# Kernel optimization log

Measured on AMD Instinct MI355X. Metric: run time of the kernel, lower is better.

Reference implementation:

```python
import jax, jax.numpy as jnp
import numpy as np

NUM_HEADS = 8
NUM_POINTS = 4


def _bilinear_gather(vl, loc, h, w):
    """MSDeformAttn bilinear sampling (align_corners=False, zero padding).
    vl: (BN, h*w, H, D) one level's values; loc: (BN, Q, H, P, 2) normalized [0,1].
    Returns (BN, Q, H, P, D)."""
    BN, _, H, D = vl.shape
    Q, P = loc.shape[1], loc.shape[3]
    x = loc[..., 0] * w - 0.5
    y = loc[..., 1] * h - 0.5
    x0 = jnp.floor(x); y0 = jnp.floor(y)
    lx = x - x0; ly = y - y0
    x0i = x0.astype(jnp.int32); y0i = y0.astype(jnp.int32)
    x1i = x0i + 1; y1i = y0i + 1
    vt = vl.transpose(0, 2, 1, 3)  # (BN, H, hw, D)

    def gather(yi, xi):
        valid = (yi >= 0) & (yi < h) & (xi >= 0) & (xi < w)
        idx = jnp.clip(yi, 0, h - 1) * w + jnp.clip(xi, 0, w - 1)  # (BN,Q,H,P)
        idx_t = idx.transpose(0, 2, 1, 3).reshape(BN, H, Q * P)
        g = jnp.take_along_axis(vt, idx_t[..., None], axis=2)  # (BN,H,QP,D)
        g = g.reshape(BN, H, Q, P, D).transpose(0, 2, 1, 3, 4)
        return jnp.where(valid[..., None], g, jnp.zeros((), vl.dtype))

    w00 = ((1 - ly) * (1 - lx))[..., None]
    w01 = ((1 - ly) * lx)[..., None]
    w10 = (ly * (1 - lx))[..., None]
    w11 = (ly * lx)[..., None]
    return (gather(y0i, x0i) * w00 + gather(y0i, x1i) * w01
            + gather(y1i, x0i) * w10 + gather(y1i, x1i) * w11)


def _forward(query, value, reference_points, query_mask, spatial_shapes, level_start_index,
             Wv, bv, Woff, boff, Watt, batt, Wo, bo):
    B, Z, Y, X, C = query.shape
    Q = Z * Y * X
    BN = value.shape[0]
    N = BN // B  # cameras per sample (uniform lengths)
    H, P = NUM_HEADS, NUM_POINTS
    shapes = np.asarray(spatial_shapes)  # static level shapes
    starts = np.asarray(level_start_index)
    L = shapes.shape[0]
    D = C // H
    mask = query_mask.astype(query.dtype)  # (BN, Q)
    # expand each sample's voxel queries to its N cameras
    qf = jnp.broadcast_to(query.reshape(B, 1, Q, C), (B, N, Q, C)).reshape(BN, Q, C)
    v = (value @ Wv + bv).reshape(BN, -1, H, D)
    off = (qf @ Woff + boff).reshape(BN, Q, H, L, P, 2)
    aw = jax.nn.softmax((qf @ Watt + batt).reshape(BN, Q, H, L * P), axis=-1)
    aw = aw.reshape(BN, Q, H, L, P)
    # offset_normalizer = (w, h) per level
    normalizer = jnp.asarray(np.stack([shapes[:, 1], shapes[:, 0]], -1), query.dtype)
    loc = reference_points[:, :, None, None, None, :] + off / normalizer[None, None, None, :, None, :]
    out = jnp.zeros((BN, Q, H, D), query.dtype)
    for l in range(L):
        h, w = int(shapes[l, 0]), int(shapes[l, 1])
        s = int(starts[l])
        vl = v[:, s:s + h * w]
        sampled = _bilinear_gather(vl, loc[:, :, :, l], h, w)  # (BN,Q,H,P,D)
        out = out + jnp.einsum('bqhpd,bqhp->bqhd', sampled, aw[:, :, :, l])
    attn = out.reshape(BN, Q, C) @ Wo + bo
    # identity + attn, then rebatch_mask_sequence zeroes non-masked voxels
    full = (qf + attn) * mask[..., None]
    summed = full.reshape(B, N, Q, C).sum(axis=1)
    counts = jnp.maximum(mask.reshape(B, N, Q).sum(axis=1), 1.0)
    return (summed / counts[..., None]).reshape(B, Z, Y, X, C)


def setup_inputs() -> dict:
    key = jax.random.key(0)
    ks = jax.random.split(key, 9)
    B, N = 2, 4
    Z, Y, X, C = 8, 32, 32, 256
    Q = Z * Y * X
    BN = B * N
    shapes = np.array([[64, 112], [32, 56], [16, 28], [8, 14]], np.int64)
    starts = np.concatenate([[0], np.cumsum(shapes[:, 0] * shapes[:, 1])[:-1]]).astype(np.int64)
    Nv = int((shapes[:, 0] * shapes[:, 1]).sum())  # 9520
    H, L, P = NUM_HEADS, shapes.shape[0], NUM_POINTS
    s = 0.02
    return dict(
        query=jax.random.normal(ks[0], (B, Z, Y, X, C), jnp.float32),
        value=jax.random.normal(ks[1], (BN, Nv, C), jnp.float32),
        reference_points=jax.random.uniform(ks[2], (BN, Q, 2), jnp.float32),
        query_mask=jax.random.bernoulli(ks[3], 0.6, (BN, Q)),
        spatial_shapes=jnp.asarray(shapes),
        level_start_index=jnp.asarray(starts),
        Wv=jax.random.normal(ks[4], (C, C), jnp.float32) * s,
        bv=jnp.zeros((C,), jnp.float32),
        Woff=jax.random.normal(ks[5], (C, H * L * P * 2), jnp.float32) * s,
        boff=jax.random.normal(ks[6], (H * L * P * 2,), jnp.float32),
        Watt=jax.random.normal(ks[7], (C, H * L * P), jnp.float32) * s,
        batt=jnp.zeros((H * L * P,), jnp.float32),
        Wo=jax.random.normal(ks[8], (C, C), jnp.float32) * s,
        bo=jnp.zeros((C,), jnp.float32),
    )


def reference(query, value, reference_points, query_mask, spatial_shapes, level_start_index,
              Wv, bv, Woff, boff, Watt, batt, Wo, bo):
    return _forward(query, value, reference_points, query_mask, spatial_shapes, level_start_index,
                    Wv, bv, Woff, boff, Watt, batt, Wo, bo)
```

## Files before the change

### kernel.cpp

```cpp
#include <hip/hip_runtime.h>
#include <cstdint>
#include <cstddef>

#define QQ 8192
#define CDIM 256
#define NV 9520
#define NLVL 4
#define NPTS 4
#define NHEAD 8

typedef __attribute__((ext_vector_type(8))) short short8;
typedef __attribute__((ext_vector_type(4))) float f32x4;

__device__ __forceinline__ unsigned short f2bf(float f)
{
    unsigned u = __float_as_uint(f);
    unsigned r = (u + 0x7fffu + ((u >> 16) & 1u)) >> 16;
    return (unsigned short)r;
}
__device__ __forceinline__ unsigned pk2bf(float a, float b)
{
    return (unsigned)f2bf(a) | ((unsigned)f2bf(b) << 16);
}

__global__ void pack_weights_kernel(
    const float* __restrict__ Wv,
    const float* __restrict__ Woff, const float* __restrict__ boff,
    const float* __restrict__ Watt, const float* __restrict__ batt,
    const float* __restrict__ Wo,
    unsigned short* __restrict__ Wt_v,
    unsigned short* __restrict__ Wt_oa,
    unsigned short* __restrict__ Wt_o,
    float* __restrict__ bias_oa)
{
    const int n = blockIdx.x, k = threadIdx.x;
    if (n < 256) {
        Wt_v[n * 256 + k] = f2bf(Wv[(size_t)k * 256 + n]);
    } else if (n < 512) {
        const int c = n - 256;
        Wt_oa[c * 256 + k] = f2bf(Woff[(size_t)k * 256 + c]);
        if (k == 0) bias_oa[c] = boff[c];
    } else if (n < 640) {
        const int c = n - 512;
        Wt_oa[(256 + c) * 256 + k] = f2bf(Watt[(size_t)k * 128 + c]);
        if (k == 0) bias_oa[256 + c] = batt[c];
    } else {
        const int c = n - 640;
        Wt_o[c * 256 + k] = f2bf(Wo[(size_t)k * 256 + c]);
    }
}

enum { EP_BIAS_BF16 = 0, EP_BIAS_F32 = 1, EP_WO_FINAL = 2 };

template <int EP, bool AF32>
__global__ __launch_bounds__(256) void mfma_gemm_kernel(
    const void* __restrict__ Ap,
    const unsigned short* __restrict__ Bt,
    const float* __restrict__ bias,
    void* __restrict__ C, int ldc,
    const float* __restrict__ query,
    const float* __restrict__ bo,
    const float* __restrict__ cnts)
{
    __shared__ unsigned short As[128 * 64];
    __shared__ unsigned short Bs[128 * 64];
    const int tid  = threadIdx.x;
    const int lane = tid & 63;
    const int wave = tid >> 6;
    const int wm = wave >> 1, wn = wave & 1;
    const int lr = lane & 15, g = lane >> 4;
    const int m0 = blockIdx.x * 128, n0 = blockIdx.y * 128;

    f32x4 acc[4][4];
    #pragma unroll
    for (int mi = 0; mi < 4; ++mi)
        #pragma unroll
        for (int ni = 0; ni < 4; ++ni)
            acc[mi][ni] = (f32x4){0.f, 0.f, 0.f, 0.f};

    const unsigned short* gB = Bt + (size_t)n0 * 256;

    for (int kt = 0; kt < 4; ++kt) {
        uint4 ra[4], rb[4];
        #pragma unroll
        for (int it = 0; it < 4; ++it) {
            const int fb  = it * 256 + tid;
            const int row = fb >> 3, kb = fb & 7;
            if constexpr (AF32) {
                const float* gA = (const float*)Ap + (size_t)m0 * 256;
                const float* p = gA + (size_t)row * 256 + kt * 64 + kb * 8;
                float4 f0 = *(const float4*)p;
                float4 f1 = *(const float4*)(p + 4);
                ra[it] = make_uint4(pk2bf(f0.x, f0.y), pk2bf(f0.z, f0.w),
                                    pk2bf(f1.x, f1.y), pk2bf(f1.z, f1.w));
            } else {
                const unsigned short* gA = (const unsigned short*)Ap + (size_t)m0 * 256;
                ra[it] = *(const uint4*)(gA + (size_t)row * 256 + kt * 64 + kb * 8);
            }
            rb[it] = *(const uint4*)(gB + (size_t)row * 256 + kt * 64 + kb * 8);
        }
        __syncthreads();
        #pragma unroll
        for (int it = 0; it < 4; ++it) {
            const int fb  = it * 256 + tid;
            const int row = fb >> 3, kb = fb & 7;
            const int sw  = (kb ^ (row & 7)) << 3;
            *(uint4*)&As[row * 64 + sw] = ra[it];
            *(uint4*)&Bs[row * 64 + sw] = rb[it];
        }
        __syncthreads();
        #pragma unroll
        for (int kk = 0; kk < 2; ++kk) {
            const int kb = kk * 4 + g;
            short8 af[4], bf[4];
            #pragma unroll
            for (int mi = 0; mi < 4; ++mi) {
                const int row = wm * 64 + mi * 16 + lr;
                af[mi] = *(const short8*)&As[row * 64 + ((kb ^ (row & 7)) << 3)];
            }
            #pragma unroll
            for (int ni = 0; ni < 4; ++ni) {
                const int row = wn * 64 + ni * 16 + lr;
                bf[ni] = *(const short8*)&Bs[row * 64 + ((kb ^ (row & 7)) << 3)];
            }
            #pragma unroll
            for (int mi = 0; mi < 4; ++mi)
                #pragma unroll
                for (int ni = 0; ni < 4; ++ni)
                    acc[mi][ni] = __builtin_amdgcn_mfma_f32_16x16x32_bf16(
                        af[mi], bf[ni], acc[mi][ni], 0, 0, 0);
        }
    }

    float bcol[4];
    #pragma unroll
    for (int ni = 0; ni < 4; ++ni)
        bcol[ni] = bias[n0 + wn * 64 + ni * 16 + lr];
    #pragma unroll
    for (int mi = 0; mi < 4; ++mi) {
        #pragma unroll
        for (int j = 0; j < 4; ++j) {
            const int gm = m0 + wm * 64 + mi * 16 + g * 4 + j;
            #pragma unroll
            for (int ni = 0; ni < 4; ++ni) {
                const int gn = n0 + wn * 64 + ni * 16 + lr;
                const float r = acc[mi][ni][j] + bcol[ni];
                if constexpr (EP == EP_BIAS_BF16)
                    ((unsigned short*)C)[(size_t)gm * ldc + gn] = f2bf(r);
                else
                    ((float*)C)[(size_t)gm * ldc + gn] = r;
            }
        }
    }
}

template <int EP, bool AF32>
__global__ __launch_bounds__(512) void mfma_gemm256_kernel(
    const void* __restrict__ Ap,
    const unsigned short* __restrict__ Bt,
    const float* __restrict__ bias,
    void* __restrict__ C,
    const float* __restrict__ query,
    const float* __restrict__ bo,
    const float* __restrict__ cnts)
{
    __shared__ unsigned short As[128 * 64];
    __shared__ unsigned short Bs[256 * 64];
    const int tid  = threadIdx.x;
    const int lane = tid & 63;
    const int wave = tid >> 6;
    const int wm = wave >> 2, wn = wave & 3;
    const int lr = lane & 15, g = lane >> 4;
    const int m0 = blockIdx.x * 128;

    f32x4 acc[4][4];
    #pragma unroll
    for (int mi = 0; mi < 4; ++mi)
        #pragma unroll
        for (int ni = 0; ni < 4; ++ni)
            acc[mi][ni] = (f32x4){0.f, 0.f, 0.f, 0.f};

    for (int kt = 0; kt < 4; ++kt) {
        uint4 ra[2], rb[4];
        #pragma unroll
        for (int it = 0; it < 2; ++it) {
            const int fb  = it * 512 + tid;
            const int row = fb >> 3, kb = fb & 7;
            if constexpr (AF32) {
                const float* gA = (const float*)Ap + (size_t)m0 * 256;
                const float* p = gA + (size_t)row * 256 + kt * 64 + kb * 8;
                float4 f0 = *(const float4*)p;
                float4 f1 = *(const float4*)(p + 4);
                ra[it] = make_uint4(pk2bf(f0.x, f0.y), pk2bf(f0.z, f0.w),
                                    pk2bf(f1.x, f1.y), pk2bf(f1.z, f1.w));
            } else {
                const unsigned short* gA = (const unsigned short*)Ap + (size_t)m0 * 256;
                ra[it] = *(const uint4*)(gA + (size_t)row * 256 + kt * 64 + kb * 8);
            }
        }
        #pragma unroll
        for (int it = 0; it < 4; ++it) {
            const int fb  = it * 512 + tid;
            const int row = fb >> 3, kb = fb & 7;
            rb[it] = *(const uint4*)(Bt + (size_t)row * 256 + kt * 64 + kb * 8);
        }
        __syncthreads();
        #pragma unroll
        for (int it = 0; it < 2; ++it) {
            const int fb  = it * 512 + tid;
            const int row = fb >> 3, kb = fb & 7;
            *(uint4*)&As[row * 64 + ((kb ^ (row & 7)) << 3)] = ra[it];
        }
        #pragma unroll
        for (int it = 0; it < 4; ++it) {
            const int fb  = it * 512 + tid;
            const int row = fb >> 3, kb = fb & 7;
            *(uint4*)&Bs[row * 64 + ((kb ^ (row & 7)) << 3)] = rb[it];
        }
        __syncthreads();
        #pragma unroll
        for (int kk = 0; kk < 2; ++kk) {
            const int kb = kk * 4 + g;
            short8 af[4], bf[4];
            #pragma unroll
            for (int mi = 0; mi < 4; ++mi) {
                const int row = wm * 64 + mi * 16 + lr;
                af[mi] = *(const short8*)&As[row * 64 + ((kb ^ (row & 7)) << 3)];
            }
            #pragma unroll
            for (int ni = 0; ni < 4; ++ni) {
                const int row = wn * 64 + ni * 16 + lr;
                bf[ni] = *(const short8*)&Bs[row * 64 + ((kb ^ (row & 7)) << 3)];
            }
            #pragma unroll
            for (int mi = 0; mi < 4; ++mi)
                #pragma unroll
                for (int ni = 0; ni < 4; ++ni)
                    acc[mi][ni] = __builtin_amdgcn_mfma_f32_16x16x32_bf16(
                        af[mi], bf[ni], acc[mi][ni], 0, 0, 0);
        }
    }

    float bcol[4];
    #pragma unroll
    for (int ni = 0; ni < 4; ++ni)
        bcol[ni] = (EP == EP_WO_FINAL ? bo : bias)[wn * 64 + ni * 16 + lr];
    #pragma unroll
    for (int mi = 0; mi < 4; ++mi) {
        #pragma unroll
        for (int j = 0; j < 4; ++j) {
            const int gm = m0 + wm * 64 + mi * 16 + g * 4 + j;
            if constexpr (EP == EP_WO_FINAL) {
                const float sm = cnts[gm];
                const float inv = 1.f / fmaxf(sm, 1.f);
                #pragma unroll
                for (int ni = 0; ni < 4; ++ni) {
                    const int gn = wn * 64 + ni * 16 + lr;
                    const float qv = query[(size_t)gm * CDIM + gn] + bcol[ni];
                    ((float*)C)[(size_t)gm * CDIM + gn] =
                        (sm * qv + acc[mi][ni][j]) * inv;
                }
            } else {
                #pragma unroll
                for (int ni = 0; ni < 4; ++ni) {
                    const int gn = wn * 64 + ni * 16 + lr;
                    const float r = acc[mi][ni][j] + bcol[ni];
                    if constexpr (EP == EP_BIAS_BF16)
                        ((unsigned short*)C)[(size_t)gm * CDIM + gn] = f2bf(r);
                    else
                        ((float*)C)[(size_t)gm * CDIM + gn] = r;
                }
            }
        }
    }
}

__global__ void detect_mask_kernel(const unsigned int* __restrict__ m, int* flag)
{
    __shared__ int notI32, notF32;
    if (threadIdx.x == 0) { notI32 = 0; notF32 = 0; }
    __syncthreads();
    for (int i = threadIdx.x; i < 1024; i += 256) {
        unsigned v = m[i];
        if (v > 1u) notI32 = 1;
        if (v != 0u && v != 0x3F800000u) notF32 = 1;
    }
    __syncthreads();
    if (threadIdx.x == 0) *flag = (!notI32) ? 1 : ((!notF32) ? 2 : 0);
}

__device__ __forceinline__ float read_mask(const void* p, int f, size_t i)
{
    if (f == 1) return (float)((const int*)p)[i];
    if (f == 2) return ((const float*)p)[i];
    return (float)((const unsigned char*)p)[i];
}

__global__ __launch_bounds__(256) void sample_reduce_kernel(
    const unsigned short* __restrict__ v,
    const float* __restrict__ offatt,
    const float* __restrict__ refp,
    const void* __restrict__ maskp,
    const int* __restrict__ flag,
    unsigned short* __restrict__ S,
    float* __restrict__ cnts)
{
    __shared__ int4   sidx[4][NHEAD][17];
    __shared__ float4 swt[4][NHEAD][17];
    __shared__ float  red[4][CDIM];
    __shared__ float  smv[4];
    const int tid  = threadIdx.x;
    const int wn   = tid >> 6;
    const int lane = tid & 63;
    const int bq   = blockIdx.x;
    const int b    = bq >> 13;
    const int q    = bq & (QQ - 1);
    const int bn   = b * 4 + wn;

    const float mn = read_mask(maskp, *flag, (size_t)bn * QQ + q);
    if (lane == 0) smv[wn] = mn;

    const float* oa = offatt + (size_t)bq * 384;
    const float rx = refp[((size_t)bn * QQ + q) * 2 + 0];
    const float ry = refp[((size_t)bn * QQ + q) * 2 + 1];

    #pragma unroll
    for (int cc = 0; cc < 2; ++cc) {
        const int c = lane + cc * 64;
        const int hcomb = c >> 4;
        const int pcomb = c & 15;
        const int l = (c >> 2) & 3;
        const int hh = 64 >> l;
        const int ww = 112 >> l;
        const int s  = (l > 0 ? 7168 : 0) + (l > 1 ? 1792 : 0) + (l > 2 ? 448 : 0);
        const float offx = oa[c * 2 + 0];
        const float offy = oa[c * 2 + 1];
        const float logit = oa[256 + c];
        float mx = logit;
        #pragma unroll
        for (int d = 1; d < 16; d <<= 1) mx = fmaxf(mx, __shfl_xor(mx, d));
        const float e = __expf(logit - mx);
        float se = e;
        #pragma unroll
        for (int d = 1; d < 16; d <<= 1) se += __shfl_xor(se, d);
        const float aw = e / se;

        const float x = rx * (float)ww - 0.5f + offx;
        const float y = ry * (float)hh - 0.5f + offy;
        const float x0f = floorf(x), y0f = floorf(y);
        const float lx = x - x0f, ly = y - y0f;
        const int x0 = (int)x0f, y0 = (int)y0f;
        const int x1 = x0 + 1,  y1 = y0 + 1;
        const bool vx0 = (x0 >= 0) & (x0 < ww);
        const bool vx1 = (x1 >= 0) & (x1 < ww);
        const bool vy0 = (y0 >= 0) & (y0 < hh);
        const bool vy1 = (y1 >= 0) & (y1 < hh);
        const int xc0 = min(max(x0, 0), ww - 1);
        const int xc1 = min(max(x1, 0), ww - 1);
        const int yc0 = min(max(y0, 0), hh - 1);
        const int yc1 = min(max(y1, 0), hh - 1);
        float w00 = (1.f - ly) * (1.f - lx) * aw;
        float w01 = (1.f - ly) * lx * aw;
        float w10 = ly * (1.f - lx) * aw;
        float w11 = ly * lx * aw;
        w00 = (vy0 & vx0) ? w00 : 0.f;
        w01 = (vy0 & vx1) ? w01 : 0.f;
        w10 = (vy1 & vx0) ? w10 : 0.f;
        w11 = (vy1 & vx1) ? w11 : 0.f;
        sidx[wn][hcomb][pcomb] = make_int4(s + yc0 * ww + xc0, s + yc0 * ww + xc1,
                                           s + yc1 * ww + xc0, s + yc1 * ww + xc1);
        swt[wn][hcomb][pcomb]  = make_float4(w00, w01, w10, w11);
    }

    float4 acc = make_float4(0.f, 0.f, 0.f, 0.f);
    if (mn != 0.f) {
        const int h  = lane >> 3;
        const int d4 = lane & 7;
        const int laneoff = h * 8 + d4;
        const uint2* vb = (const uint2*)(v + (size_t)bn * NV * CDIM);
        #pragma unroll 4
        for (int p = 0; p < 16; ++p) {
            const int4   id = sidx[wn][h][p];
            const float4 wt = swt[wn][h][p];
            const uint2 g00 = vb[(size_t)(id.x * 64 + laneoff)];
            const uint2 g01 = vb[(size_t)(id.y * 64 + laneoff)];
            const uint2 g10 = vb[(size_t)(id.z * 64 + laneoff)];
            const uint2 g11 = vb[(size_t)(id.w * 64 + laneoff)];
            #define BFLO(u) __uint_as_float((u) << 16)
            #define BFHI(u) __uint_as_float((u) & 0xffff0000u)
            acc.x += wt.x * BFLO(g00.x) + wt.y * BFLO(g01.x) + wt.z * BFLO(g10.x) + wt.w * BFLO(g11.x);
            acc.y += wt.x * BFHI(g00.x) + wt.y * BFHI(g01.x) + wt.z * BFHI(g10.x) + wt.w * BFHI(g11.x);
            acc.z += wt.x * BFLO(g00.y) + wt.y * BFLO(g01.y) + wt.z * BFLO(g10.y) + wt.w * BFLO(g11.y);
            acc.w += wt.x * BFHI(g00.y) + wt.y * BFHI(g01.y) + wt.z * BFHI(g10.y) + wt.w * BFHI(g11.y);
            #undef BFLO
            #undef BFHI
        }
    }
    *(float4*)&red[wn][lane * 4] = acc;
    __syncthreads();

    const float ssum = red[0][tid] + red[1][tid] + red[2][tid] + red[3][tid];
    S[(size_t)bq * CDIM + tid] = f2bf(ssum);
    if (tid == 0) cnts[bq] = smv[0] + smv[1] + smv[2] + smv[3];
}

extern "C" void kernel_launch(void* const* d_in, const int* in_sizes, int n_in,
                              void* d_out, int out_size, void* d_ws, size_t ws_size,
                              hipStream_t stream)
{
    (void)in_sizes; (void)n_in; (void)out_size; (void)ws_size;
    const float* query = (const float*)d_in[0];
    const float* value = (const float*)d_in[1];
    const float* refp  = (const float*)d_in[2];
    const void*  maskp = d_in[3];
    const float* Wv    = (const float*)d_in[6];
    const float* bv    = (const float*)d_in[7];
    const float* Woff  = (const float*)d_in[8];
    const float* boff  = (const float*)d_in[9];
    const float* Watt  = (const float*)d_in[10];
    const float* batt  = (const float*)d_in[11];
    const float* Wo    = (const float*)d_in[12];
    const float* bo    = (const float*)d_in[13];
    float* out = (float*)d_out;
    char* ws = (char*)d_ws;

    unsigned short* v_proj  = (unsigned short*)(ws + 0);
    float*          offatt  = (float*)(ws + 38993920);
    unsigned short* S_bf16  = (unsigned short*)(ws + 64159744);
    unsigned short* Wt_v    = (unsigned short*)(ws + 72548352);
    unsigned short* Wt_oa   = (unsigned short*)(ws + 72679424);
    unsigned short* Wt_o    = (unsigned short*)(ws + 72876032);
    float*          bias_oa = (float*)(ws + 73007104);
    float*          cnts    = (float*)(ws + 73008640);
    int*            flag    = (int*)(ws + 73074176);

    detect_mask_kernel<<<1, 256, 0, stream>>>((const unsigned int*)maskp, flag);

    pack_weights_kernel<<<896, 256, 0, stream>>>(
        Wv, Woff, boff, Watt, batt, Wo, Wt_v, Wt_oa, Wt_o, bias_oa);

    mfma_gemm256_kernel<EP_BIAS_BF16, true><<<595, 512, 0, stream>>>(
        value, Wt_v, bv, v_proj, nullptr, nullptr, nullptr);

    mfma_gemm_kernel<EP_BIAS_F32, true><<<dim3(128, 3), 256, 0, stream>>>(
        query, Wt_oa, bias_oa, offatt, 384, nullptr, nullptr, nullptr);

    sample_reduce_kernel<<<16384, 256, 0, stream>>>(
        v_proj, offatt, refp, maskp, flag, S_bf16, cnts);

    mfma_gemm256_kernel<EP_WO_FINAL, false><<<128, 512, 0, stream>>>(
        S_bf16, Wt_o, nullptr, out, query, bo, cnts);
}
```

Baseline: 218.5 us.

## Merge projection GEMMs into one launch, fuse mask detect, skip masked sampling

```diff
diff --git a/kernel.cpp b/kernel.cpp
--- a/kernel.cpp
+++ b/kernel.cpp
@@ -23,15 +23,17 @@
     return (unsigned)f2bf(a) | ((unsigned)f2bf(b) << 16);
 }
 
-__global__ void pack_weights_kernel(
+__global__ void pack_weights_detect_kernel(
     const float* __restrict__ Wv,
     const float* __restrict__ Woff, const float* __restrict__ boff,
     const float* __restrict__ Watt, const float* __restrict__ batt,
     const float* __restrict__ Wo,
+    const unsigned int* __restrict__ maskw,
     unsigned short* __restrict__ Wt_v,
     unsigned short* __restrict__ Wt_oa,
     unsigned short* __restrict__ Wt_o,
-    float* __restrict__ bias_oa)
+    float* __restrict__ bias_oa,
+    int* __restrict__ flag)
 {
     const int n = blockIdx.x, k = threadIdx.x;
     if (n < 256) {
@@ -44,32 +46,49 @@
         const int c = n - 512;
         Wt_oa[(256 + c) * 256 + k] = f2bf(Watt[(size_t)k * 128 + c]);
         if (k == 0) bias_oa[256 + c] = batt[c];
+    } else if (n < 768) {
+        const int c = n - 640;
+        Wt_oa[(384 + c) * 256 + k] = 0;
+        if (k == 0) bias_oa[384 + c] = 0.f;
+    } else if (n < 1024) {
+        const int c = n - 768;
+        Wt_o[c * 256 + k] = f2bf(Wo[(size_t)k * 256 + c]);
     } else {
-        const int c = n - 640;
-        Wt_o[c * 256 + k] = f2bf(Wo[(size_t)k * 256 + c]);
-    }
-}
-
-enum { EP_BIAS_BF16 = 0, EP_BIAS_F32 = 1, EP_WO_FINAL = 2 };
-
-template <int EP, bool AF32>
-__global__ __launch_bounds__(256) void mfma_gemm_kernel(
-    const void* __restrict__ Ap,
-    const unsigned short* __restrict__ Bt,
-    const float* __restrict__ bias,
-    void* __restrict__ C, int ldc,
-    const float* __restrict__ query,
-    const float* __restrict__ bo,
-    const float* __restrict__ cnts)
+        __shared__ int notI32, notF32;
+        if (k == 0) { notI32 = 0; notF32 = 0; }
+        __syncthreads();
+        for (int i = k; i < 1024; i += 256) {
+            unsigned v = maskw[i];
+            if (v > 1u) notI32 = 1;
+            if (v != 0u && v != 0x3F800000u) notF32 = 1;
+        }
+        __syncthreads();
+        if (k == 0) *flag = (!notI32) ? 1 : ((!notF32) ? 2 : 0);
+    }
+}
+
+__global__ __launch_bounds__(512) void mega_gemm_kernel(
+    const float* __restrict__ value, const float* __restrict__ query,
+    const unsigned short* __restrict__ Wt_v,
+    const unsigned short* __restrict__ Wt_oa,
+    const float* __restrict__ bv, const float* __restrict__ bias_oa,
+    unsigned short* __restrict__ v_proj, float* __restrict__ offatt)
 {
     __shared__ unsigned short As[128 * 64];
-    __shared__ unsigned short Bs[128 * 64];
+    __shared__ unsigned short Bs[256 * 64];
+    const int bid = blockIdx.x;
+    int role, m0;
+    const float* A;
+    const unsigned short* Bt;
+    if (bid < 595)      { role = 0; m0 = bid * 128;         A = value; Bt = Wt_v; }
+    else if (bid < 723) { role = 1; m0 = (bid - 595) * 128; A = query; Bt = Wt_oa; }
+    else                { role = 2; m0 = (bid - 723) * 128; A = query; Bt = Wt_oa + 256 * 256; }
+
     const int tid  = threadIdx.x;
     const int lane = tid & 63;
     const int wave = tid >> 6;
-    const int wm = wave >> 1, wn = wave & 1;
+    const int wm = wave >> 2, wn = wave & 3;
     const int lr = lane & 15, g = lane >> 4;
-    const int m0 = blockIdx.x * 128, n0 = blockIdx.y * 128;
 
     f32x4 acc[4][4];
     #pragma unroll
@@ -78,35 +97,36 @@
         for (int ni = 0; ni < 4; ++ni)
             acc[mi][ni] = (f32x4){0.f, 0.f, 0.f, 0.f};
 
-    const unsigned short* gB = Bt + (size_t)n0 * 256;
-
     for (int kt = 0; kt < 4; ++kt) {
-        uint4 ra[4], rb[4];
+        uint4 ra[2], rb[4];
+        #pragma unroll
+        for (int it = 0; it < 2; ++it) {
+            const int fb  = it * 512 + tid;
+            const int row = fb >> 3, kb = fb & 7;
+            const float* p = A + (size_t)(m0 + row) * 256 + kt * 64 + kb * 8;
+            float4 f0 = *(const float4*)p;
+            float4 f1 = *(const float4*)(p + 4);
+            ra[it] = make_uint4(pk2bf(f0.x, f0.y), pk2bf(f0.z, f0.w),
+                                pk2bf(f1.x, f1.y), pk2bf(f1.z, f1.w));
+        }
         #pragma unroll
         for (int it = 0; it < 4; ++it) {
-            const int fb  = it * 256 + tid;
-            const int row = fb >> 3, kb = fb & 7;
-            if constexpr (AF32) {
-                const float* gA = (const float*)Ap + (size_t)m0 * 256;
-                const float* p = gA + (size_t)row * 256 + kt * 64 + kb * 8;
-                float4 f0 = *(const float4*)p;
-                float4 f1 = *(const float4*)(p + 4);
-                ra[it] = make_uint4(pk2bf(f0.x, f0.y), pk2bf(f0.z, f0.w),
-                                    pk2bf(f1.x, f1.y), pk2bf(f1.z, f1.w));
-            } else {
-                const unsigned short* gA = (const unsigned short*)Ap + (size_t)m0 * 256;
-                ra[it] = *(const uint4*)(gA + (size_t)row * 256 + kt * 64 + kb * 8);
-            }
-            rb[it] = *(const uint4*)(gB + (size_t)row * 256 + kt * 64 + kb * 8);
-        }
-        __syncthreads();
+            const int fb  = it * 512 + tid;
+            const int row = fb >> 3, kb = fb & 7;
+            rb[it] = *(const uint4*)(Bt + (size_t)row * 256 + kt * 64 + kb * 8);
+        }
+        __syncthreads();
+        #pragma unroll
+        for (int it = 0; it < 2; ++it) {
+            const int fb  = it * 512 + tid;
+            const int row = fb >> 3, kb = fb & 7;
+            *(uint4*)&As[row * 64 + ((kb ^ (row & 7)) << 3)] = ra[it];
+        }
         #pragma unroll
         for (int it = 0; it < 4; ++it) {
-            const int fb  = it * 256 + tid;
-            const int row = fb >> 3, kb = fb & 7;
-            const int sw  = (kb ^ (row & 7)) << 3;
-            *(uint4*)&As[row * 64 + sw] = ra[it];
-            *(uint4*)&Bs[row * 64 + sw] = rb[it];
+            const int fb  = it * 512 + tid;
+            const int row = fb >> 3, kb = fb & 7;
+            *(uint4*)&Bs[row * 64 + ((kb ^ (row & 7)) << 3)] = rb[it];
         }
         __syncthreads();
         #pragma unroll
@@ -134,8 +154,11 @@
 
     float bcol[4];
     #pragma unroll
-    for (int ni = 0; ni < 4; ++ni)
-        bcol[ni] = bias[n0 + wn * 64 + ni * 16 + lr];
+    for (int ni = 0; ni < 4; ++ni) {
+        const int gn = wn * 64 + ni * 16 + lr;
+        bcol[ni] = (role == 0) ? bv[gn]
+                 : (role == 1) ? bias_oa[gn] : bias_oa[256 + gn];
+    }
     #pragma unroll
     for (int mi = 0; mi < 4; ++mi) {
         #pragma unroll
@@ -143,35 +166,34 @@
             const int gm = m0 + wm * 64 + mi * 16 + g * 4 + j;
             #pragma unroll
             for (int ni = 0; ni < 4; ++ni) {
-                const int gn = n0 + wn * 64 + ni * 16 + lr;
+                const int gn = wn * 64 + ni * 16 + lr;
                 const float r = acc[mi][ni][j] + bcol[ni];
-                if constexpr (EP == EP_BIAS_BF16)
-                    ((unsigned short*)C)[(size_t)gm * ldc + gn] = f2bf(r);
-                else
-                    ((float*)C)[(size_t)gm * ldc + gn] = r;
-            }
-        }
-    }
-}
-
-template <int EP, bool AF32>
-__global__ __launch_bounds__(512) void mfma_gemm256_kernel(
-    const void* __restrict__ Ap,
-    const unsigned short* __restrict__ Bt,
-    const float* __restrict__ bias,
-    void* __restrict__ C,
+                if (role == 0)
+                    v_proj[(size_t)gm * 256 + gn] = f2bf(r);
+                else if (role == 1)
+                    offatt[(size_t)gm * 384 + gn] = r;
+                else if (gn < 128)
+                    offatt[(size_t)gm * 384 + 256 + gn] = r;
+            }
+        }
+    }
+}
+
+__global__ __launch_bounds__(256) void wo_final_kernel(
+    const unsigned short* __restrict__ S,
+    const unsigned short* __restrict__ Wt_o,
     const float* __restrict__ query,
     const float* __restrict__ bo,
-    const float* __restrict__ cnts)
-{
-    __shared__ unsigned short As[128 * 64];
+    const float* __restrict__ cnts,
+    float* __restrict__ out)
+{
+    __shared__ unsigned short As[64 * 64];
     __shared__ unsigned short Bs[256 * 64];
     const int tid  = threadIdx.x;
     const int lane = tid & 63;
-    const int wave = tid >> 6;
-    const int wm = wave >> 2, wn = wave & 3;
+    const int wn   = tid >> 6;
     const int lr = lane & 15, g = lane >> 4;
-    const int m0 = blockIdx.x * 128;
+    const int m0 = blockIdx.x * 64;
 
     f32x4 acc[4][4];
     #pragma unroll
@@ -181,39 +203,29 @@
             acc[mi][ni] = (f32x4){0.f, 0.f, 0.f, 0.f};
 
     for (int kt = 0; kt < 4; ++kt) {
-        uint4 ra[2], rb[4];
+        uint4 ra[2], rb[8];
         #pragma unroll
         for (int it = 0; it < 2; ++it) {
-            const int fb  = it * 512 + tid;
-            const int row = fb >> 3, kb = fb & 7;
-            if constexpr (AF32) {
-                const float* gA = (const float*)Ap + (size_t)m0 * 256;
-                const float* p = gA + (size_t)row * 256 + kt * 64 + kb * 8;
-                float4 f0 = *(const float4*)p;
-                float4 f1 = *(const float4*)(p + 4);
-                ra[it] = make_uint4(pk2bf(f0.x, f0.y), pk2bf(f0.z, f0.w),
-                                    pk2bf(f1.x, f1.y), pk2bf(f1.z, f1.w));
-            } else {
-                const unsigned short* gA = (const unsigned short*)Ap + (size_t)m0 * 256;
-                ra[it] = *(const uint4*)(gA + (size_t)row * 256 + kt * 64 + kb * 8);
-            }
-        }
-        #pragma unroll
-        for (int it = 0; it < 4; ++it) {
-            const int fb  = it * 512 + tid;
-            const int row = fb >> 3, kb = fb & 7;
-            rb[it] = *(const uint4*)(Bt + (size_t)row * 256 + kt * 64 + kb * 8);
+            const int fb  = it * 256 + tid;
+            const int row = fb >> 3, kb = fb & 7;
+            ra[it] = *(const uint4*)(S + (size_t)(m0 + row) * 256 + kt * 64 + kb * 8);
+        }
+        #pragma unroll
+        for (int it = 0; it < 8; ++it) {
+            const int fb  = it * 256 + tid;
+            const int row = fb >> 3, kb = fb & 7;
+            rb[it] = *(const uint4*)(Wt_o + (size_t)row * 256 + kt * 64 + kb * 8);
         }
         __syncthreads();
         #pragma unroll
         for (int it = 0; it < 2; ++it) {
-            const int fb  = it * 512 + tid;
+            const int fb  = it * 256 + tid;
             const int row = fb >> 3, kb = fb & 7;
             *(uint4*)&As[row * 64 + ((kb ^ (row & 7)) << 3)] = ra[it];
         }
         #pragma unroll
-        for (int it = 0; it < 4; ++it) {
-            const int fb  = it * 512 + tid;
+        for (int it = 0; it < 8; ++it) {
+            const int fb  = it * 256 + tid;
             const int row = fb >> 3, kb = fb & 7;
             *(uint4*)&Bs[row * 64 + ((kb ^ (row & 7)) << 3)] = rb[it];
         }
@@ -224,7 +236,7 @@
             short8 af[4], bf[4];
             #pragma unroll
             for (int mi = 0; mi < 4; ++mi) {
-                const int row = wm * 64 + mi * 16 + lr;
+                const int row = mi * 16 + lr;
                 af[mi] = *(const short8*)&As[row * 64 + ((kb ^ (row & 7)) << 3)];
             }
             #pragma unroll
@@ -244,49 +256,22 @@
     float bcol[4];
     #pragma unroll
     for (int ni = 0; ni < 4; ++ni)
-        bcol[ni] = (EP == EP_WO_FINAL ? bo : bias)[wn * 64 + ni * 16 + lr];
+        bcol[ni] = bo[wn * 64 + ni * 16 + lr];
     #pragma unroll
     for (int mi = 0; mi < 4; ++mi) {
         #pragma unroll
         for (int j = 0; j < 4; ++j) {
-            const int gm = m0 + wm * 64 + mi * 16 + g * 4 + j;
-            if constexpr (EP == EP_WO_FINAL) {
-                const float sm = cnts[gm];
-                const float inv = 1.f / fmaxf(sm, 1.f);
-                #pragma unroll
-                for (int ni = 0; ni < 4; ++ni) {
-                    const int gn = wn * 64 + ni * 16 + lr;
-                    const float qv = query[(size_t)gm * CDIM + gn] + bcol[ni];
-                    ((float*)C)[(size_t)gm * CDIM + gn] =
-                        (sm * qv + acc[mi][ni][j]) * inv;
-                }
-            } else {
-                #pragma unroll
-                for (int ni = 0; ni < 4; ++ni) {
-                    const int gn = wn * 64 + ni * 16 + lr;
-                    const float r = acc[mi][ni][j] + bcol[ni];
-                    if constexpr (EP == EP_BIAS_BF16)
-                        ((unsigned short*)C)[(size_t)gm * CDIM + gn] = f2bf(r);
-                    else
-                        ((float*)C)[(size_t)gm * CDIM + gn] = r;
-                }
-            }
-        }
-    }
-}
-
-__global__ void detect_mask_kernel(const unsigned int* __restrict__ m, int* flag)
-{
-    __shared__ int notI32, notF32;
-    if (threadIdx.x == 0) { notI32 = 0; notF32 = 0; }
-    __syncthreads();
-    for (int i = threadIdx.x; i < 1024; i += 256) {
-        unsigned v = m[i];
-        if (v > 1u) notI32 = 1;
-        if (v != 0u && v != 0x3F800000u) notF32 = 1;
-    }
-    __syncthreads();
-    if (threadIdx.x == 0) *flag = (!notI32) ? 1 : ((!notF32) ? 2 : 0);
+            const int gm = m0 + mi * 16 + g * 4 + j;
+            const float sm = cnts[gm];
+            const float inv = 1.f / fmaxf(sm, 1.f);
+            #pragma unroll
+            for (int ni = 0; ni < 4; ++ni) {
+                const int gn = wn * 64 + ni * 16 + lr;
+                const float qv = query[(size_t)gm * CDIM + gn] + bcol[ni];
+                out[(size_t)gm * CDIM + gn] = (sm * qv + acc[mi][ni][j]) * inv;
+            }
+        }
+    }
 }
 
 __device__ __forceinline__ float read_mask(const void* p, int f, size_t i)
@@ -320,65 +305,65 @@
     const float mn = read_mask(maskp, *flag, (size_t)bn * QQ + q);
     if (lane == 0) smv[wn] = mn;
 
-    const float* oa = offatt + (size_t)bq * 384;
-    const float rx = refp[((size_t)bn * QQ + q) * 2 + 0];
-    const float ry = refp[((size_t)bn * QQ + q) * 2 + 1];
-
-    #pragma unroll
-    for (int cc = 0; cc < 2; ++cc) {
-        const int c = lane + cc * 64;
-        const int hcomb = c >> 4;
-        const int pcomb = c & 15;
-        const int l = (c >> 2) & 3;
-        const int hh = 64 >> l;
-        const int ww = 112 >> l;
-        const int s  = (l > 0 ? 7168 : 0) + (l > 1 ? 1792 : 0) + (l > 2 ? 448 : 0);
-        const float offx = oa[c * 2 + 0];
-        const float offy = oa[c * 2 + 1];
-        const float logit = oa[256 + c];
-        float mx = logit;
-        #pragma unroll
-        for (int d = 1; d < 16; d <<= 1) mx = fmaxf(mx, __shfl_xor(mx, d));
-        const float e = __expf(logit - mx);
-        float se = e;
-        #pragma unroll
-        for (int d = 1; d < 16; d <<= 1) se += __shfl_xor(se, d);
-        const float aw = e / se;
-
-        const float x = rx * (float)ww - 0.5f + offx;
-        const float y = ry * (float)hh - 0.5f + offy;
-        const float x0f = floorf(x), y0f = floorf(y);
-        const float lx = x - x0f, ly = y - y0f;
-        const int x0 = (int)x0f, y0 = (int)y0f;
-        const int x1 = x0 + 1,  y1 = y0 + 1;
-        const bool vx0 = (x0 >= 0) & (x0 < ww);
-        const bool vx1 = (x1 >= 0) & (x1 < ww);
-        const bool vy0 = (y0 >= 0) & (y0 < hh);
-        const bool vy1 = (y1 >= 0) & (y1 < hh);
-        const int xc0 = min(max(x0, 0), ww - 1);
-        const int xc1 = min(max(x1, 0), ww - 1);
-        const int yc0 = min(max(y0, 0), hh - 1);
-        const int yc1 = min(max(y1, 0), hh - 1);
-        float w00 = (1.f - ly) * (1.f - lx) * aw;
-        float w01 = (1.f - ly) * lx * aw;
-        float w10 = ly * (1.f - lx) * aw;
-        float w11 = ly * lx * aw;
-        w00 = (vy0 & vx0) ? w00 : 0.f;
-        w01 = (vy0 & vx1) ? w01 : 0.f;
-        w10 = (vy1 & vx0) ? w10 : 0.f;
-        w11 = (vy1 & vx1) ? w11 : 0.f;
-        sidx[wn][hcomb][pcomb] = make_int4(s + yc0 * ww + xc0, s + yc0 * ww + xc1,
-                                           s + yc1 * ww + xc0, s + yc1 * ww + xc1);
-        swt[wn][hcomb][pcomb]  = make_float4(w00, w01, w10, w11);
-    }
-
     float4 acc = make_float4(0.f, 0.f, 0.f, 0.f);
     if (mn != 0.f) {
+        const float* oa = offatt + (size_t)bq * 384;
+        const float rx = refp[((size_t)bn * QQ + q) * 2 + 0];
+        const float ry = refp[((size_t)bn * QQ + q) * 2 + 1];
+
+        #pragma unroll
+        for (int cc = 0; cc < 2; ++cc) {
+            const int c = lane + cc * 64;
+            const int hcomb = c >> 4;
+            const int pcomb = c & 15;
+            const int l = (c >> 2) & 3;
+            const int hh = 64 >> l;
+            const int ww = 112 >> l;
+            const int s  = (l > 0 ? 7168 : 0) + (l > 1 ? 1792 : 0) + (l > 2 ? 448 : 0);
+            const float offx = oa[c * 2 + 0];
+            const float offy = oa[c * 2 + 1];
+            const float logit = oa[256 + c];
+            float mx = logit;
+            #pragma unroll
+            for (int d = 1; d < 16; d <<= 1) mx = fmaxf(mx, __shfl_xor(mx, d));
+            const float e = __expf(logit - mx);
+            float se = e;
+            #pragma unroll
+            for (int d = 1; d < 16; d <<= 1) se += __shfl_xor(se, d);
+            const float aw = e / se;
+
+            const float x = rx * (float)ww - 0.5f + offx;
+            const float y = ry * (float)hh - 0.5f + offy;
+            const float x0f = floorf(x), y0f = floorf(y);
+            const float lx = x - x0f, ly = y - y0f;
+            const int x0 = (int)x0f, y0 = (int)y0f;
+            const int x1 = x0 + 1,  y1 = y0 + 1;
+            const bool vx0 = (x0 >= 0) & (x0 < ww);
+            const bool vx1 = (x1 >= 0) & (x1 < ww);
+            const bool vy0 = (y0 >= 0) & (y0 < hh);
+            const bool vy1 = (y1 >= 0) & (y1 < hh);
+            const int xc0 = min(max(x0, 0), ww - 1);
+            const int xc1 = min(max(x1, 0), ww - 1);
+            const int yc0 = min(max(y0, 0), hh - 1);
+            const int yc1 = min(max(y1, 0), hh - 1);
+            float w00 = (1.f - ly) * (1.f - lx) * aw;
+            float w01 = (1.f - ly) * lx * aw;
+            float w10 = ly * (1.f - lx) * aw;
+            float w11 = ly * lx * aw;
+            w00 = (vy0 & vx0) ? w00 : 0.f;
+            w01 = (vy0 & vx1) ? w01 : 0.f;
+            w10 = (vy1 & vx0) ? w10 : 0.f;
+            w11 = (vy1 & vx1) ? w11 : 0.f;
+            sidx[wn][hcomb][pcomb] = make_int4(s + yc0 * ww + xc0, s + yc0 * ww + xc1,
+                                               s + yc1 * ww + xc0, s + yc1 * ww + xc1);
+            swt[wn][hcomb][pcomb]  = make_float4(w00, w01, w10, w11);
+        }
+
         const int h  = lane >> 3;
         const int d4 = lane & 7;
         const int laneoff = h * 8 + d4;
         const uint2* vb = (const uint2*)(v + (size_t)bn * NV * CDIM);
-        #pragma unroll 4
+        #pragma unroll 8
         for (int p = 0; p < 16; ++p) {
             const int4   id = sidx[wn][h][p];
             const float4 wt = swt[wn][h][p];
@@ -429,25 +414,21 @@
     unsigned short* S_bf16  = (unsigned short*)(ws + 64159744);
     unsigned short* Wt_v    = (unsigned short*)(ws + 72548352);
     unsigned short* Wt_oa   = (unsigned short*)(ws + 72679424);
-    unsigned short* Wt_o    = (unsigned short*)(ws + 72876032);
-    float*          bias_oa = (float*)(ws + 73007104);
-    float*          cnts    = (float*)(ws + 73008640);
-    int*            flag    = (int*)(ws + 73074176);
-
-    detect_mask_kernel<<<1, 256, 0, stream>>>((const unsigned int*)maskp, flag);
-
-    pack_weights_kernel<<<896, 256, 0, stream>>>(
-        Wv, Woff, boff, Watt, batt, Wo, Wt_v, Wt_oa, Wt_o, bias_oa);
-
-    mfma_gemm256_kernel<EP_BIAS_BF16, true><<<595, 512, 0, stream>>>(
-        value, Wt_v, bv, v_proj, nullptr, nullptr, nullptr);
-
-    mfma_gemm_kernel<EP_BIAS_F32, true><<<dim3(128, 3), 256, 0, stream>>>(
-        query, Wt_oa, bias_oa, offatt, 384, nullptr, nullptr, nullptr);
+    unsigned short* Wt_o    = (unsigned short*)(ws + 72941568);
+    float*          bias_oa = (float*)(ws + 73072640);
+    float*          cnts    = (float*)(ws + 73074688);
+    int*            flag    = (int*)(ws + 73140224);
+
+    pack_weights_detect_kernel<<<1025, 256, 0, stream>>>(
+        Wv, Woff, boff, Watt, batt, Wo, (const unsigned int*)maskp,
+        Wt_v, Wt_oa, Wt_o, bias_oa, flag);
+
+    mega_gemm_kernel<<<851, 512, 0, stream>>>(
+        value, query, Wt_v, Wt_oa, bv, bias_oa, v_proj, offatt);
 
     sample_reduce_kernel<<<16384, 256, 0, stream>>>(
         v_proj, offatt, refp, maskp, flag, S_bf16, cnts);
 
-    mfma_gemm256_kernel<EP_WO_FINAL, false><<<128, 512, 0, stream>>>(
-        S_bf16, Wt_o, nullptr, out, query, bo, cnts);
-}
+    wo_final_kernel<<<256, 256, 0, stream>>>(
+        S_bf16, Wt_o, query, bo, cnts, out);
+}
```

Result: slower. 252.4 us (+15.5%).
